# Kernel optimization log

Hardware: AMD Instinct MI355X
Metric: run time of the kernel (lower is better)

Reference implementation:

```python
import jax, jax.numpy as jnp
import numpy as np

N_NODES = 50000
N_EDGES = 800000
IN_F = 128
HID = 16
HEADS = 8
OUT_F = 128


def setup_inputs() -> dict:
    key = jax.random.key(0)
    ks = jax.random.split(key, 16)
    h = jax.random.normal(ks[0], (N_NODES, IN_F), dtype=jnp.float32)
    src1 = jax.random.randint(ks[1], (N_EDGES,), 0, N_NODES, dtype=jnp.int32)
    dst1 = jax.random.randint(ks[2], (N_EDGES,), 0, N_NODES, dtype=jnp.int32)
    src2 = jax.random.randint(ks[3], (N_EDGES,), 0, N_NODES, dtype=jnp.int32)
    dst2 = jax.random.randint(ks[4], (N_EDGES,), 0, N_NODES, dtype=jnp.int32)
    norm1 = jax.random.uniform(ks[5], (N_NODES, 1), dtype=jnp.float32)
    norm2 = jax.random.uniform(ks[6], (N_NODES, 1), dtype=jnp.float32)
    D = HEADS * HID  # 128
    W_lin = jax.random.normal(ks[7], (IN_F, D), dtype=jnp.float32) * (1.0 / np.sqrt(IN_F))
    b_lin = jax.random.normal(ks[8], (D,), dtype=jnp.float32) * 0.01
    al = jax.random.normal(ks[9], (HEADS, HID, 1), dtype=jnp.float32) * 0.1
    ar = jax.random.normal(ks[10], (HEADS, HID, 1), dtype=jnp.float32) * 0.1
    W_fc = jax.random.normal(ks[11], (D, OUT_F), dtype=jnp.float32) * (1.0 / np.sqrt(D))
    b_fc = jax.random.normal(ks[12], (OUT_F,), dtype=jnp.float32) * 0.01
    return {"h": h, "src1": src1, "dst1": dst1, "src2": src2, "dst2": dst2,
            "norm1": norm1, "norm2": norm2, "W_lin": W_lin, "b_lin": b_lin,
            "al": al, "ar": ar, "W_fc": W_fc, "b_fc": b_fc}


def _propagate(feat, norm, src, dst, n_nodes):
    # msg = h[src] * norm[src]; accum[v] = sum_{e: dst=v} msg_e; out = accum * norm
    msg = feat[src] * norm[src]                      # [E, D]
    agg = jax.ops.segment_sum(msg, dst, num_segments=n_nodes)
    return agg * norm                                # [N, D]


def _leaky_relu(x):
    return jnp.where(x > 0, x, 0.2 * x)


def reference(h, src1, dst1, src2, dst2, norm1, norm2, W_lin, b_lin, al, ar, W_fc, b_fc):
    N = h.shape[0]
    hf = h @ W_lin + b_lin                           # [N, 8*HID] (dropout p given but eval-mode -> identity)
    h1 = _propagate(hf, norm1, src1, dst1, N)
    h2 = _propagate(hf, norm2, src2, dst2, N)
    # Faithful to torch: row-major reshape [N, 8*HID] -> (8, N, HID)
    h1r = h1.reshape(HEADS, N, HID)
    h2r = h2.reshape(HEADS, N, HID)
    hr = hf.reshape(HEADS, N, HID)
    ai = jnp.einsum('hnd,hdo->hno', hr, al)          # [8, N, 1]
    aj1 = jnp.einsum('hnd,hdo->hno', h1r, ar)
    aj2 = jnp.einsum('hnd,hdo->hno', h2r, ar)
    a1 = jnp.clip(jnp.exp(_leaky_relu(ai + aj1)), -10.0, 10.0)
    a2 = jnp.clip(jnp.exp(_leaky_relu(ai + aj2)), -10.0, 10.0)
    denom = a1 + a2
    out = (a1 / denom) * h1r + (a2 / denom) * h2r    # [8, N, HID]
    out = out.reshape(N, HEADS * HID)
    return out @ W_fc + b_fc
```

## Files before the change

kernel.cpp:

```cpp
#include <hip/hip_runtime.h>

#define NN 50000
#define NE 800000
#define NB 196
#define NBG 392
#define NBLK 128
#define CHUNK 6250
#define MAXB 6144

typedef __bf16 bf16x8 __attribute__((ext_vector_type(8)));
typedef float  f32x4  __attribute__((ext_vector_type(4)));

__device__ __forceinline__ unsigned short f2bf(float x) {
    unsigned u = __float_as_uint(x);
    return (unsigned short)((u + 0x7FFFu + ((u >> 16) & 1u)) >> 16);
}
__device__ __forceinline__ float bflo(unsigned u) { return __uint_as_float(u << 16); }
__device__ __forceinline__ float bfhi(unsigned u) { return __uint_as_float(u & 0xFFFF0000u); }

__global__ __launch_bounds__(1024) void histA_kernel(
    const int* __restrict__ dst1, const int* __restrict__ dst2, int* __restrict__ histG,
    const float* __restrict__ Wa, const float* __restrict__ Wb,
    unsigned short* __restrict__ Wta, unsigned short* __restrict__ Wtb)
{
    const int t = threadIdx.x, blk = blockIdx.x;
    if (blk >= NBLK) {
        const float* W = (blk - NBLK) ? Wb : Wa;
        unsigned short* Wt = (blk - NBLK) ? Wtb : Wta;
        for (int j = t; j < 128 * 128; j += 1024) {
            int n = j >> 7, k = j & 127;
            Wt[j] = f2bf(W[k * 128 + n]);
        }
        return;
    }
    __shared__ int h[NBG];
    for (int i = t; i < NBG; i += 1024) h[i] = 0;
    __syncthreads();
    const int base = blk * CHUNK;
    for (int i = t; i < CHUNK; i += 1024) {
        atomicAdd(&h[dst1[base + i] >> 8], 1);
        atomicAdd(&h[NB + (dst2[base + i] >> 8)], 1);
    }
    __syncthreads();
    for (int i = t; i < NBG; i += 1024)
        histG[blk * NBG + i] = h[i];
}

__global__ __launch_bounds__(1024) void scatterC_kernel(
    const int* __restrict__ src1, const int* __restrict__ dst1,
    const int* __restrict__ src2, const int* __restrict__ dst2,
    const int* __restrict__ histG,
    int* __restrict__ gbbase, int* __restrict__ gbtot,
    unsigned int* __restrict__ bin1, unsigned int* __restrict__ bin2)
{
    __shared__ int s[512];
    __shared__ int pos[NBG];
    const int t = threadIdx.x, blk = blockIdx.x;

    int total_i = 0, pref_i = 0;
    if (t < NBG) {
        for (int c = 0; c < NBLK; c++) {
            int v = histG[c * NBG + t];
            total_i += v;
            if (c < blk) pref_i += v;
        }
    }
    if (t < 512) s[t] = (t < NBG) ? total_i : 0;
    __syncthreads();
    for (int off = 1; off < 512; off <<= 1) {
        int x = 0;
        if (t < 512 && t >= off) x = s[t - off];
        __syncthreads();
        if (t < 512) s[t] += x;
        __syncthreads();
    }
    const int sumG1 = s[NB - 1];
    if (t < NBG) {
        int excl = s[t] - total_i;
        int bb = excl - ((t >= NB) ? sumG1 : 0);
        pos[t] = bb + pref_i;
        if (blk == 0) { gbbase[t] = bb; gbtot[t] = total_i; }
    }
    __syncthreads();

    const int base = blk * CHUNK;
    for (int i = t; i < CHUNK; i += 1024) {
        int d = dst1[base + i], sv = src1[base + i];
        int slot = atomicAdd(&pos[d >> 8], 1);
        bin1[slot] = ((unsigned)(d & 255) << 16) | (unsigned)sv;
        d = dst2[base + i]; sv = src2[base + i];
        slot = atomicAdd(&pos[NB + (d >> 8)], 1);
        bin2[slot] = ((unsigned)(d & 255) << 16) | (unsigned)sv;
    }
}

__global__ __launch_bounds__(256) void bucket_sort_kernel(
    const unsigned int* __restrict__ bin1, const unsigned int* __restrict__ bin2,
    const int* __restrict__ bbase, const int* __restrict__ btot,
    unsigned short* __restrict__ csr1, int* __restrict__ start1, int* __restrict__ deg1,
    unsigned short* __restrict__ csr2, int* __restrict__ start2, int* __restrict__ deg2)
{
    __shared__ int lcnt[256];
    __shared__ int sc[256];
    __shared__ int oat[256];
    __shared__ unsigned short outb[MAXB];
    const int t = threadIdx.x;
    const int g = (blockIdx.x >= NB) ? 1 : 0;
    const int b = blockIdx.x - g * NB;
    const unsigned int* bin = g ? bin2 : bin1;
    unsigned short* csr = g ? csr2 : csr1;
    int* start = g ? start2 : start1;
    int* deg   = g ? deg2 : deg1;

    const int base = bbase[g * NB + b];
    const int tot = min(btot[g * NB + b], MAXB);

    lcnt[t] = 0;
    __syncthreads();
    for (int i = t; i < tot; i += 256) atomicAdd(&lcnt[bin[base + i] >> 16], 1);
    __syncthreads();
    sc[t] = lcnt[t];
    __syncthreads();
    for (int off = 1; off < 256; off <<= 1) {
        int x = (t >= off) ? sc[t - off] : 0;
        __syncthreads();
        sc[t] += x;
        __syncthreads();
    }
    const int ex = sc[t] - lcnt[t];
    oat[t] = ex;
    __syncthreads();
    for (int i = t; i < tot; i += 256) {
        unsigned v = bin[base + i];
        int slot = atomicAdd(&oat[v >> 16], 1);
        outb[slot] = (unsigned short)(v & 0xFFFFu);
    }
    __syncthreads();
    for (int i = t; i < tot; i += 256) csr[base + i] = outb[i];
    int nd = b * 256 + t;
    if (nd < NN) { start[nd] = base + ex; deg[nd] = lcnt[t]; }
}

__global__ __launch_bounds__(256) void mfma_gemm_kernel(
    const float* __restrict__ X, const unsigned short* __restrict__ Wt,
    const float* __restrict__ bias, float* __restrict__ Y,
    unsigned short* __restrict__ Ybf, int nrows)
{
    __shared__ unsigned short Wl[128 * 128];
    const int t = threadIdx.x;
    const int lane = t & 63;
    const int wv = t >> 6;
    const int row0 = blockIdx.x * 64;
    const int m16 = lane & 15;
    const int quad = lane >> 4;

    {
        const uint4* Wg = (const uint4*)Wt;
        #pragma unroll
        for (int i = 0; i < 8; i++) {
            int gi = t + i * 256;
            int n = gi >> 4, g = gi & 15;
            uint4 v = Wg[gi];
            *(uint4*)&Wl[n * 128 + (((g ^ (n & 15)) << 3))] = v;
        }
    }

    const int arow = row0 + wv * 16 + m16;
    const bool valid = (arow < nrows);
    const float4* X4 = (const float4*)X;
    float4 xr[8];
    #pragma unroll
    for (int kc = 0; kc < 4; kc++) {
        if (valid) {
            int gidx = arow * 32 + kc * 8 + quad * 2;
            xr[kc * 2]     = X4[gidx];
            xr[kc * 2 + 1] = X4[gidx + 1];
        } else {
            xr[kc * 2] = xr[kc * 2 + 1] = make_float4(0.f, 0.f, 0.f, 0.f);
        }
    }
    __syncthreads();

    f32x4 acc[8];
    #pragma unroll
    for (int nt = 0; nt < 8; nt++) acc[nt] = (f32x4){0.f, 0.f, 0.f, 0.f};

    #pragma unroll
    for (int kc = 0; kc < 4; kc++) {
        union { unsigned short u[8]; bf16x8 v; } ah, al;
        float f[8] = { xr[kc*2].x, xr[kc*2].y, xr[kc*2].z, xr[kc*2].w,
                       xr[kc*2+1].x, xr[kc*2+1].y, xr[kc*2+1].z, xr[kc*2+1].w };
        #pragma unroll
        for (int j = 0; j < 8; j++) {
            unsigned u = __float_as_uint(f[j]);
            ah.u[j] = (unsigned short)(u >> 16);
            al.u[j] = f2bf(f[j] - __uint_as_float(u & 0xFFFF0000u));
        }
        const int sgbase = (kc * 4 + quad);
        #pragma unroll
        for (int nt = 0; nt < 8; nt++) {
            const int n = nt * 16 + m16;
            bf16x8 b = *(const bf16x8*)&Wl[n * 128 + ((sgbase ^ m16) << 3)];
            acc[nt] = __builtin_amdgcn_mfma_f32_16x16x32_bf16(ah.v, b, acc[nt], 0, 0, 0);
            acc[nt] = __builtin_amdgcn_mfma_f32_16x16x32_bf16(al.v, b, acc[nt], 0, 0, 0);
        }
    }

    #pragma unroll
    for (int nt = 0; nt < 8; nt++) {
        const int col = nt * 16 + m16;
        const float bc = bias[col];
        #pragma unroll
        for (int r = 0; r < 4; r++) {
            int row = row0 + wv * 16 + quad * 4 + r;
            if (row < nrows) {
                float val = acc[nt][r] + bc;
                if (Y)   Y[(long)row * 128 + col] = val;
                if (Ybf) Ybf[(long)row * 128 + col] = f2bf(val);
            }
        }
    }
}

__global__ __launch_bounds__(256) void mfma_gemm_bf16_kernel(
    const unsigned short* __restrict__ Xbf, const unsigned short* __restrict__ Wt,
    const float* __restrict__ bias, float* __restrict__ Y, int nrows)
{
    __shared__ unsigned short Wl[128 * 128];
    const int t = threadIdx.x;
    const int lane = t & 63;
    const int wv = t >> 6;
    const int row0 = blockIdx.x * 64;
    const int m16 = lane & 15;
    const int quad = lane >> 4;

    {
        const uint4* Wg = (const uint4*)Wt;
        #pragma unroll
        for (int i = 0; i < 8; i++) {
            int gi = t + i * 256;
            int n = gi >> 4, g = gi & 15;
            uint4 v = Wg[gi];
            *(uint4*)&Wl[n * 128 + (((g ^ (n & 15)) << 3))] = v;
        }
    }

    const int arow = row0 + wv * 16 + m16;
    const bool valid = (arow < nrows);
    const uint4* X16 = (const uint4*)Xbf;
    union { uint4 u; bf16x8 v; } xr[4];
    #pragma unroll
    for (int kc = 0; kc < 4; kc++) {
        if (valid) xr[kc].u = X16[arow * 16 + kc * 4 + quad];
        else       xr[kc].u = make_uint4(0, 0, 0, 0);
    }
    __syncthreads();

    f32x4 acc[8];
    #pragma unroll
    for (int nt = 0; nt < 8; nt++) acc[nt] = (f32x4){0.f, 0.f, 0.f, 0.f};

    #pragma unroll
    for (int kc = 0; kc < 4; kc++) {
        const int sgbase = (kc * 4 + quad);
        #pragma unroll
        for (int nt = 0; nt < 8; nt++) {
            const int n = nt * 16 + m16;
            bf16x8 b = *(const bf16x8*)&Wl[n * 128 + ((sgbase ^ m16) << 3)];
            acc[nt] = __builtin_amdgcn_mfma_f32_16x16x32_bf16(xr[kc].v, b, acc[nt], 0, 0, 0);
        }
    }

    #pragma unroll
    for (int nt = 0; nt < 8; nt++) {
        const int col = nt * 16 + m16;
        const float bc = bias[col];
        #pragma unroll
        for (int r = 0; r < 4; r++) {
            int row = row0 + wv * 16 + quad * 4 + r;
            if (row < nrows) Y[(long)row * 128 + col] = acc[nt][r] + bc;
        }
    }
}

__global__ __launch_bounds__(256) void gather_attn_kernel(
    const unsigned int* __restrict__ hfb,
    const unsigned short* __restrict__ csr1, const int* __restrict__ start1,
    const int* __restrict__ deg1, const float* __restrict__ norm1,
    const unsigned short* __restrict__ csr2, const int* __restrict__ start2,
    const int* __restrict__ deg2, const float* __restrict__ norm2,
    const float* __restrict__ al, const float* __restrict__ ar,
    unsigned int* __restrict__ outb)
{
    const int lane = threadIdx.x & 63;
    int node = (blockIdx.x * 256 + threadIdx.x) >> 6;
    if (node >= NN) return;
    node = __builtin_amdgcn_readfirstlane(node);

    float2 acc1 = make_float2(0.f, 0.f), acc2 = make_float2(0.f, 0.f);

    #pragma unroll 1
    for (int g = 0; g < 2; g++) {
        const unsigned short* csr = g ? csr2 : csr1;
        const int* startp = g ? start2 : start1;
        const int* degp   = g ? deg2 : deg1;
        const float* norm = g ? norm2 : norm1;
        float2 acc = make_float2(0.f, 0.f);
        const int st = startp[node], dg = degp[node];
        for (int base = 0; base < dg; base += 64) {
            const int nb = min(64, dg - base);
            int myc = (lane < nb) ? (int)csr[st + base + lane] : 0;
            int j = 0;
            for (; j + 8 <= nb; j += 8) {
                int s[8]; float n[8]; unsigned u[8];
                #pragma unroll
                for (int q = 0; q < 8; q++) s[q] = __builtin_amdgcn_readlane(myc, j + q);
                #pragma unroll
                for (int q = 0; q < 8; q++) {
                    n[q] = norm[s[q]];
                    u[q] = hfb[(long)s[q] * 64 + lane];
                }
                #pragma unroll
                for (int q = 0; q < 8; q++) {
                    acc.x = fmaf(bflo(u[q]), n[q], acc.x);
                    acc.y = fmaf(bfhi(u[q]), n[q], acc.y);
                }
            }
            for (; j < nb; j++) {
                int s = __builtin_amdgcn_readlane(myc, j);
                float nv = norm[s];
                unsigned u = hfb[(long)s * 64 + lane];
                acc.x = fmaf(bflo(u), nv, acc.x);
                acc.y = fmaf(bfhi(u), nv, acc.y);
            }
        }
        if (g) acc2 = acc; else acc1 = acc;
    }

    const float nn1 = norm1[node], nn2 = norm2[node];
    acc1.x *= nn1; acc1.y *= nn1;
    acc2.x *= nn2; acc2.y *= nn2;

    const int cc = lane >> 3;
    const int m = node * 8 + cc;
    const int head = m / NN;
    const int hid = (2 * lane) & 15;
    unsigned uf = hfb[(long)node * 64 + lane];
    const float fx = bflo(uf), fy = bfhi(uf);
    const float av0 = al[head * 16 + hid], av1 = al[head * 16 + hid + 1];
    const float rv0 = ar[head * 16 + hid], rv1 = ar[head * 16 + hid + 1];
    float s_ai = fx * av0 + fy * av1;
    float s1 = acc1.x * rv0 + acc1.y * rv1;
    float s2 = acc2.x * rv0 + acc2.y * rv1;
    s_ai += __shfl_xor(s_ai, 1); s_ai += __shfl_xor(s_ai, 2); s_ai += __shfl_xor(s_ai, 4);
    s1   += __shfl_xor(s1, 1);   s1   += __shfl_xor(s1, 2);   s1   += __shfl_xor(s1, 4);
    s2   += __shfl_xor(s2, 1);   s2   += __shfl_xor(s2, 2);   s2   += __shfl_xor(s2, 4);
    float x1 = s_ai + s1; x1 = x1 > 0.f ? x1 : 0.2f * x1;
    float x2 = s_ai + s2; x2 = x2 > 0.f ? x2 : 0.2f * x2;
    float e1 = fminf(expf(x1), 10.f);
    float e2 = fminf(expf(x2), 10.f);
    float inv = 1.f / (e1 + e2);
    float w1 = e1 * inv, w2 = e2 * inv;
    float ox = w1 * acc1.x + w2 * acc2.x;
    float oy = w1 * acc1.y + w2 * acc2.y;
    outb[(long)node * 64 + lane] = (unsigned)f2bf(ox) | ((unsigned)f2bf(oy) << 16);
}

extern "C" void kernel_launch(void* const* d_in, const int* in_sizes, int n_in,
                              void* d_out, int out_size, void* d_ws, size_t ws_size,
                              hipStream_t stream)
{
    const float* h     = (const float*)d_in[0];
    const int*   src1  = (const int*)  d_in[1];
    const int*   dst1  = (const int*)  d_in[2];
    const int*   src2  = (const int*)  d_in[3];
    const int*   dst2  = (const int*)  d_in[4];
    const float* norm1 = (const float*)d_in[5];
    const float* norm2 = (const float*)d_in[6];
    const float* W_lin = (const float*)d_in[7];
    const float* b_lin = (const float*)d_in[8];
    const float* al    = (const float*)d_in[9];
    const float* ar    = (const float*)d_in[10];
    const float* W_fc  = (const float*)d_in[11];
    const float* b_fc  = (const float*)d_in[12];
    float* out = (float*)d_out;

    unsigned short* hfb  = (unsigned short*)d_ws;
    unsigned short* outbf = hfb + (size_t)NN * 128;
    unsigned int* bin1 = (unsigned int*)(outbf + (size_t)NN * 128);
    unsigned int* bin2 = bin1 + NE;
    unsigned short* csr1 = (unsigned short*)(bin2 + NE);
    unsigned short* csr2 = csr1 + NE;
    unsigned short* WtL  = csr2 + NE;
    unsigned short* WtF  = WtL + 128 * 128;
    int* histG  = (int*)(WtF + 128 * 128);
    int* btot   = histG + NBLK * NBG;
    int* bbase  = btot + NBG;
    int* start1 = bbase + NBG;
    int* start2 = start1 + NN;
    int* deg1   = start2 + NN;
    int* deg2   = deg1 + NN;

    histA_kernel<<<NBLK + 2, 1024, 0, stream>>>(dst1, dst2, histG, W_lin, W_fc, WtL, WtF);

    mfma_gemm_kernel<<<(NN + 63) / 64, 256, 0, stream>>>(h, WtL, b_lin, nullptr, hfb, NN);

    scatterC_kernel<<<NBLK, 1024, 0, stream>>>(src1, dst1, src2, dst2, histG,
                                               bbase, btot, bin1, bin2);

    bucket_sort_kernel<<<NBG, 256, 0, stream>>>(bin1, bin2, bbase, btot,
                                                csr1, start1, deg1,
                                                csr2, start2, deg2);

    gather_attn_kernel<<<(NN * 64) / 256, 256, 0, stream>>>(
        (const unsigned int*)hfb,
        csr1, start1, deg1, norm1,
        csr2, start2, deg2, norm2,
        al, ar, (unsigned int*)outbf);

    mfma_gemm_bf16_kernel<<<(NN + 63) / 64, 256, 0, stream>>>(outbf, WtF, b_fc, out, NN);
}
```

Baseline: 229.8 us.

## Restructure gather to load 16-byte rows across four edges per wave

The per-node gather now has each quarter-wave fetch a whole 256-byte bf16 row with uint4 loads, so four edges are in flight per instruction and 32 edges are issued before any are consumed. Neighbour norms are preloaded once per lane and broadcast by shuffle instead of being scalar-loaded per edge, and partial sums are combined with cross-quarter shuffles. A fast path covers nodes with degree at most 64 and a general loop handles the rest. The aim is to cut load instruction count and raise memory-level parallelism, at the cost of more registers, more shuffles and a launch-bounds occupancy hint.

```diff
diff --git a/kernel.cpp b/kernel.cpp
--- a/kernel.cpp
+++ b/kernel.cpp
@@ -17,6 +17,9 @@
 }
 __device__ __forceinline__ float bflo(unsigned u) { return __uint_as_float(u << 16); }
 __device__ __forceinline__ float bfhi(unsigned u) { return __uint_as_float(u & 0xFFFF0000u); }
+__device__ __forceinline__ unsigned pack2(float a, float b) {
+    return (unsigned)f2bf(a) | ((unsigned)f2bf(b) << 16);
+}
 
 __global__ __launch_bounds__(1024) void histA_kernel(
     const int* __restrict__ dst1, const int* __restrict__ dst2, int* __restrict__ histG,
@@ -143,8 +146,7 @@
 
 __global__ __launch_bounds__(256) void mfma_gemm_kernel(
     const float* __restrict__ X, const unsigned short* __restrict__ Wt,
-    const float* __restrict__ bias, float* __restrict__ Y,
-    unsigned short* __restrict__ Ybf, int nrows)
+    const float* __restrict__ bias, unsigned short* __restrict__ Ybf, int nrows)
 {
     __shared__ unsigned short Wl[128 * 128];
     const int t = threadIdx.x;
@@ -213,11 +215,7 @@
         #pragma unroll
         for (int r = 0; r < 4; r++) {
             int row = row0 + wv * 16 + quad * 4 + r;
-            if (row < nrows) {
-                float val = acc[nt][r] + bc;
-                if (Y)   Y[(long)row * 128 + col] = val;
-                if (Ybf) Ybf[(long)row * 128 + col] = f2bf(val);
-            }
+            if (row < nrows) Ybf[(long)row * 128 + col] = f2bf(acc[nt][r] + bc);
         }
     }
 }
@@ -283,87 +281,145 @@
     }
 }
 
-__global__ __launch_bounds__(256) void gather_attn_kernel(
-    const unsigned int* __restrict__ hfb,
+__global__ __launch_bounds__(256, 4) void gather_attn_kernel(
+    const unsigned short* __restrict__ hfb,
     const unsigned short* __restrict__ csr1, const int* __restrict__ start1,
     const int* __restrict__ deg1, const float* __restrict__ norm1,
     const unsigned short* __restrict__ csr2, const int* __restrict__ start2,
     const int* __restrict__ deg2, const float* __restrict__ norm2,
     const float* __restrict__ al, const float* __restrict__ ar,
-    unsigned int* __restrict__ outb)
+    unsigned short* __restrict__ outb)
 {
     const int lane = threadIdx.x & 63;
-    int node = (blockIdx.x * 256 + threadIdx.x) >> 6;
-    if (node >= NN) return;
+    const int wv = threadIdx.x >> 6;
+    int node = blockIdx.x * 4 + wv;
     node = __builtin_amdgcn_readfirstlane(node);
-
-    float2 acc1 = make_float2(0.f, 0.f), acc2 = make_float2(0.f, 0.f);
-
-    #pragma unroll 1
-    for (int g = 0; g < 2; g++) {
-        const unsigned short* csr = g ? csr2 : csr1;
-        const int* startp = g ? start2 : start1;
-        const int* degp   = g ? deg2 : deg1;
-        const float* norm = g ? norm2 : norm1;
-        float2 acc = make_float2(0.f, 0.f);
-        const int st = startp[node], dg = degp[node];
-        for (int base = 0; base < dg; base += 64) {
-            const int nb = min(64, dg - base);
-            int myc = (lane < nb) ? (int)csr[st + base + lane] : 0;
-            int j = 0;
-            for (; j + 8 <= nb; j += 8) {
-                int s[8]; float n[8]; unsigned u[8];
-                #pragma unroll
-                for (int q = 0; q < 8; q++) s[q] = __builtin_amdgcn_readlane(myc, j + q);
-                #pragma unroll
-                for (int q = 0; q < 8; q++) {
-                    n[q] = norm[s[q]];
-                    u[q] = hfb[(long)s[q] * 64 + lane];
-                }
-                #pragma unroll
-                for (int q = 0; q < 8; q++) {
-                    acc.x = fmaf(bflo(u[q]), n[q], acc.x);
-                    acc.y = fmaf(bfhi(u[q]), n[q], acc.y);
+    const char* tblb = (const char*)hfb;
+    const int qtr = lane >> 4;
+    const int sub16 = (lane & 15) * 16;
+
+    const uint4 ufv = *(const uint4*)(tblb + ((long)node << 8) + sub16);
+
+    const int st1 = start1[node], dg1 = deg1[node];
+    const int st2 = start2[node], dg2 = deg2[node];
+
+#define GA_ISSUE(vv, nn_, myc, nv, j0, nb)                                 \
+    _Pragma("unroll")                                                      \
+    for (int k = 0; k < 8; k++) {                                          \
+        int e = (j0) + 4 * k + qtr;                                        \
+        int ec = (e < (nb)) ? e : 0;                                       \
+        int sx = __shfl((myc), ec);                                        \
+        float nq = __shfl((nv), ec);                                       \
+        nn_[k] = (e < (nb)) ? nq : 0.f;                                    \
+        vv[k] = *(const uint4*)(tblb + (((long)sx) << 8) + sub16);         \
+    }
+
+#define GA_CONSUME(vv, nn_, acc)                                           \
+    _Pragma("unroll")                                                      \
+    for (int k = 0; k < 8; k++) {                                          \
+        const float n = nn_[k];                                            \
+        acc[0] = fmaf(bflo(vv[k].x), n, acc[0]);                           \
+        acc[1] = fmaf(bfhi(vv[k].x), n, acc[1]);                           \
+        acc[2] = fmaf(bflo(vv[k].y), n, acc[2]);                           \
+        acc[3] = fmaf(bfhi(vv[k].y), n, acc[3]);                           \
+        acc[4] = fmaf(bflo(vv[k].z), n, acc[4]);                           \
+        acc[5] = fmaf(bfhi(vv[k].z), n, acc[5]);                           \
+        acc[6] = fmaf(bflo(vv[k].w), n, acc[6]);                           \
+        acc[7] = fmaf(bfhi(vv[k].w), n, acc[7]);                           \
+    }
+
+    float acc1[8] = {0,0,0,0,0,0,0,0}, acc2[8] = {0,0,0,0,0,0,0,0};
+
+    if (__builtin_expect(dg1 <= 64 && dg2 <= 64, 1)) {
+        int myc1 = (lane < dg1) ? (int)csr1[st1 + lane] : 0;
+        int myc2 = (lane < dg2) ? (int)csr2[st2 + lane] : 0;
+        const float nv1 = norm1[myc1];
+        const float nv2 = norm2[myc2];
+
+        uint4 vA[8], vB[8]; float nA[8], nB[8];
+        GA_ISSUE(vA, nA, myc1, nv1, 0, dg1)
+        GA_ISSUE(vB, nB, myc2, nv2, 0, dg2)
+        __builtin_amdgcn_sched_barrier(0);
+        GA_CONSUME(vA, nA, acc1)
+        GA_CONSUME(vB, nB, acc2)
+        if (dg1 > 32) {
+            GA_ISSUE(vA, nA, myc1, nv1, 32, dg1)
+            __builtin_amdgcn_sched_barrier(0);
+            GA_CONSUME(vA, nA, acc1)
+        }
+        if (dg2 > 32) {
+            GA_ISSUE(vB, nB, myc2, nv2, 32, dg2)
+            __builtin_amdgcn_sched_barrier(0);
+            GA_CONSUME(vB, nB, acc2)
+        }
+    } else {
+        #pragma unroll 1
+        for (int g = 0; g < 2; g++) {
+            const unsigned short* csr = g ? csr2 : csr1;
+            const int st = g ? st2 : st1;
+            const int dg = g ? dg2 : dg1;
+            const float* norm = g ? norm2 : norm1;
+            float* acc = g ? acc2 : acc1;
+            for (int base = 0; base < dg; base += 64) {
+                const int nb = min(64, dg - base);
+                int myc = (lane < nb) ? (int)csr[st + base + lane] : 0;
+                const float nv = norm[myc];
+                for (int j = 0; j < nb; j += 32) {
+                    uint4 vv[8]; float nn_[8];
+                    GA_ISSUE(vv, nn_, myc, nv, j, nb)
+                    __builtin_amdgcn_sched_barrier(0);
+                    GA_CONSUME(vv, nn_, acc)
                 }
             }
-            for (; j < nb; j++) {
-                int s = __builtin_amdgcn_readlane(myc, j);
-                float nv = norm[s];
-                unsigned u = hfb[(long)s * 64 + lane];
-                acc.x = fmaf(bflo(u), nv, acc.x);
-                acc.y = fmaf(bfhi(u), nv, acc.y);
-            }
-        }
-        if (g) acc2 = acc; else acc1 = acc;
+        }
+    }
+#undef GA_ISSUE
+#undef GA_CONSUME
+
+    #pragma unroll
+    for (int i = 0; i < 8; i++) {
+        acc1[i] += __shfl_xor(acc1[i], 16);
+        acc1[i] += __shfl_xor(acc1[i], 32);
+        acc2[i] += __shfl_xor(acc2[i], 16);
+        acc2[i] += __shfl_xor(acc2[i], 32);
     }
 
     const float nn1 = norm1[node], nn2 = norm2[node];
-    acc1.x *= nn1; acc1.y *= nn1;
-    acc2.x *= nn2; acc2.y *= nn2;
-
-    const int cc = lane >> 3;
-    const int m = node * 8 + cc;
-    const int head = m / NN;
-    const int hid = (2 * lane) & 15;
-    unsigned uf = hfb[(long)node * 64 + lane];
-    const float fx = bflo(uf), fy = bfhi(uf);
-    const float av0 = al[head * 16 + hid], av1 = al[head * 16 + hid + 1];
-    const float rv0 = ar[head * 16 + hid], rv1 = ar[head * 16 + hid + 1];
-    float s_ai = fx * av0 + fy * av1;
-    float s1 = acc1.x * rv0 + acc1.y * rv1;
-    float s2 = acc2.x * rv0 + acc2.y * rv1;
-    s_ai += __shfl_xor(s_ai, 1); s_ai += __shfl_xor(s_ai, 2); s_ai += __shfl_xor(s_ai, 4);
-    s1   += __shfl_xor(s1, 1);   s1   += __shfl_xor(s1, 2);   s1   += __shfl_xor(s1, 4);
-    s2   += __shfl_xor(s2, 1);   s2   += __shfl_xor(s2, 2);   s2   += __shfl_xor(s2, 4);
+
+    const int m = lane & 15;
+    const int head = (node * 8 + (m >> 1)) / NN;
+    const int hb = head * 16 + ((m & 1) << 3);
+    float uff[8] = { bflo(ufv.x), bfhi(ufv.x), bflo(ufv.y), bfhi(ufv.y),
+                     bflo(ufv.z), bfhi(ufv.z), bflo(ufv.w), bfhi(ufv.w) };
+    float s_ai = 0.f, s1 = 0.f, s2 = 0.f;
+    #pragma unroll
+    for (int i = 0; i < 8; i++) {
+        acc1[i] *= nn1;
+        acc2[i] *= nn2;
+        const float avi = al[hb + i], rvi = ar[hb + i];
+        s_ai = fmaf(uff[i], avi, s_ai);
+        s1   = fmaf(acc1[i], rvi, s1);
+        s2   = fmaf(acc2[i], rvi, s2);
+    }
+    s_ai += __shfl_xor(s_ai, 1);
+    s1   += __shfl_xor(s1, 1);
+    s2   += __shfl_xor(s2, 1);
+
     float x1 = s_ai + s1; x1 = x1 > 0.f ? x1 : 0.2f * x1;
     float x2 = s_ai + s2; x2 = x2 > 0.f ? x2 : 0.2f * x2;
     float e1 = fminf(expf(x1), 10.f);
     float e2 = fminf(expf(x2), 10.f);
     float inv = 1.f / (e1 + e2);
     float w1 = e1 * inv, w2 = e2 * inv;
-    float ox = w1 * acc1.x + w2 * acc2.x;
-    float oy = w1 * acc1.y + w2 * acc2.y;
-    outb[(long)node * 64 + lane] = (unsigned)f2bf(ox) | ((unsigned)f2bf(oy) << 16);
+
+    if (lane < 16) {
+        uint4 w;
+        w.x = pack2(w1 * acc1[0] + w2 * acc2[0], w1 * acc1[1] + w2 * acc2[1]);
+        w.y = pack2(w1 * acc1[2] + w2 * acc2[2], w1 * acc1[3] + w2 * acc2[3]);
+        w.z = pack2(w1 * acc1[4] + w2 * acc2[4], w1 * acc1[5] + w2 * acc2[5]);
+        w.w = pack2(w1 * acc1[6] + w2 * acc2[6], w1 * acc1[7] + w2 * acc2[7]);
+        *(uint4*)((char*)outb + ((long)node << 8) + m * 16) = w;
+    }
 }
 
 extern "C" void kernel_launch(void* const* d_in, const int* in_sizes, int n_in,
@@ -403,7 +459,7 @@
 
     histA_kernel<<<NBLK + 2, 1024, 0, stream>>>(dst1, dst2, histG, W_lin, W_fc, WtL, WtF);
 
-    mfma_gemm_kernel<<<(NN + 63) / 64, 256, 0, stream>>>(h, WtL, b_lin, nullptr, hfb, NN);
+    mfma_gemm_kernel<<<(NN + 63) / 64, 256, 0, stream>>>(h, WtL, b_lin, hfb, NN);
 
     scatterC_kernel<<<NBLK, 1024, 0, stream>>>(src1, dst1, src2, dst2, histG,
                                                bbase, btot, bin1, bin2);
@@ -412,11 +468,11 @@
                                                 csr1, start1, deg1,
                                                 csr2, start2, deg2);
 
-    gather_attn_kernel<<<(NN * 64) / 256, 256, 0, stream>>>(
-        (const unsigned int*)hfb,
+    gather_attn_kernel<<<12500, 256, 0, stream>>>(
+        hfb,
         csr1, start1, deg1, norm1,
         csr2, start2, deg2, norm2,
-        al, ar, (unsigned int*)outbf);
+        al, ar, outbf);
 
     mfma_gemm_bf16_kernel<<<(NN + 63) / 64, 256, 0, stream>>>(outbf, WtF, b_fc, out, NN);
 }
```

Measured after the change: 242.1 us. 1.05x slower.
